# Kernel tuning notes

Measured on AMD Instinct MI355X. Metric: run time of the kernel, lower is better.

Reference implementation:

```python
import jax, jax.numpy as jnp
import numpy as np

N = 50000      # nodes
E = 250000     # edges
NG = 2500      # graphs
H = 32         # atom_dim
ND = 32        # node feature dim
ED = 16        # edge feature dim
CONV_N = 3     # message passing steps
EMB_STEPS = 3  # Set2Set processing steps


def setup_inputs() -> dict:
    key = jax.random.key(0)
    ks = jax.random.split(key, 16)
    w = lambda k, shape, s=0.05: jax.random.normal(k, shape, jnp.float32) * s
    return {
        "x": jax.random.normal(ks[0], (N, ND), jnp.float32),
        "edge_index": jax.random.randint(ks[1], (2, E), 0, N),
        "edge_attr": jax.random.normal(ks[2], (E, ED), jnp.float32),
        "batch": jnp.sort(jax.random.randint(ks[3], (N,), 0, NG)),
        "lin_w": w(ks[4], (ND, H)), "lin_b": jnp.zeros((H,), jnp.float32),
        "e_w1": w(ks[5], (ED, 2 * H)), "e_b1": jnp.zeros((2 * H,), jnp.float32),
        "e_w2": w(ks[6], (2 * H, H * H)), "e_b2": jnp.zeros((H * H,), jnp.float32),
        "gru_w_ih": w(ks[7], (3 * H, H)), "gru_w_hh": w(ks[8], (3 * H, H)),
        "gru_b_ih": jnp.zeros((3 * H,), jnp.float32), "gru_b_hh": jnp.zeros((3 * H,), jnp.float32),
        "lstm_w_ih": w(ks[9], (4 * H, 2 * H)), "lstm_w_hh": w(ks[10], (4 * H, H)),
        "lstm_b_ih": jnp.zeros((4 * H,), jnp.float32), "lstm_b_hh": jnp.zeros((4 * H,), jnp.float32),
        "pred_w": w(ks[11], (2 * H, 1)), "pred_b": jnp.zeros((1,), jnp.float32),
    }


def _mpnn_forward(x, edge_attr, lin_w, lin_b, e_w1, e_b1, e_w2, e_b2,
                  gru_w_ih, gru_w_hh, gru_b_ih, gru_b_hh,
                  lstm_w_ih, lstm_w_hh, lstm_b_ih, lstm_b_hh,
                  pred_w, pred_b, edge_index, batch):
    src, dst = edge_index[0], edge_index[1]
    # initial node embedding: relu(Linear(node_dim -> atom_dim))
    out = jax.nn.relu(x @ lin_w + lin_b)            # [N, H]
    h = out                                         # GRU hidden state [N, H]

    # edge-conditioned weights (edge MLP output is constant across conv steps)
    e_h = jax.nn.relu(edge_attr @ e_w1 + e_b1)      # [E, 2H]
    W_e = (e_h @ e_w2 + e_b2).reshape(E, H, H)      # [E, H, H]

    # mean-aggregation denominator per target node
    deg = jax.ops.segment_sum(jnp.ones((E,), out.dtype), dst, num_segments=N)
    denom = jnp.maximum(deg, 1.0)[:, None]          # [N, 1]

    for _ in range(CONV_N):
        # NNConv message: m_e = x_src @ W_e, mean-scattered to dst
        msg = jnp.einsum('eh,eho->eo', out[src], W_e)                   # [E, H]
        agg = jax.ops.segment_sum(msg, dst, num_segments=N) / denom     # [N, H]
        m = jax.nn.relu(agg)
        # single GRU cell step (seq_len=1)
        gi = m @ gru_w_ih.T + gru_b_ih              # [N, 3H]
        gh = h @ gru_w_hh.T + gru_b_hh              # [N, 3H]
        i_r, i_z, i_n = jnp.split(gi, 3, axis=-1)
        h_r, h_z, h_n = jnp.split(gh, 3, axis=-1)
        r = jax.nn.sigmoid(i_r + h_r)
        z = jax.nn.sigmoid(i_z + h_z)
        n = jnp.tanh(i_n + r * h_n)
        h = (1.0 - z) * n + z * h
        out = h

    # Set2Set pooling over graphs (only last embedding used, residual='last')
    q_star = jnp.zeros((NG, 2 * H), out.dtype)
    hl = jnp.zeros((NG, H), out.dtype)
    cl = jnp.zeros((NG, H), out.dtype)
    for _ in range(EMB_STEPS):
        g = q_star @ lstm_w_ih.T + lstm_b_ih + hl @ lstm_w_hh.T + lstm_b_hh  # [NG, 4H]
        gi_, gf_, gg_, go_ = jnp.split(g, 4, axis=-1)
        i_g = jax.nn.sigmoid(gi_)
        f_g = jax.nn.sigmoid(gf_)
        g_g = jnp.tanh(gg_)
        o_g = jax.nn.sigmoid(go_)
        cl = f_g * cl + i_g * g_g
        hl = o_g * jnp.tanh(cl)
        q = hl                                       # [NG, H]
        e = jnp.sum(out * q[batch], axis=-1)         # [N]
        e_max = jax.ops.segment_max(e, batch, num_segments=NG)
        e_exp = jnp.exp(e - e_max[batch])
        e_den = jax.ops.segment_sum(e_exp, batch, num_segments=NG)
        a = e_exp / e_den[batch]                     # softmax within each graph
        r_pool = jax.ops.segment_sum(a[:, None] * out, batch, num_segments=NG)  # [NG, H]
        q_star = jnp.concatenate([q, r_pool], axis=-1)

    pred = q_star @ pred_w + pred_b                  # [NG, 1]
    return pred.reshape(-1)


def reference(x, edge_index, edge_attr, batch, lin_w, lin_b, e_w1, e_b1, e_w2, e_b2,
              gru_w_ih, gru_w_hh, gru_b_ih, gru_b_hh,
              lstm_w_ih, lstm_w_hh, lstm_b_ih, lstm_b_hh, pred_w, pred_b):
    return _mpnn_forward(x, edge_attr, lin_w, lin_b, e_w1, e_b1, e_w2, e_b2,
                         gru_w_ih, gru_w_hh, gru_b_ih, gru_b_hh,
                         lstm_w_ih, lstm_w_hh, lstm_b_ih, lstm_b_hh,
                         pred_w, pred_b, edge_index, batch)
```

## Files before the change

### kernel.cpp

```cpp
#include <hip/hip_runtime.h>
#include <hip/hip_bf16.h>

namespace {
constexpr int kN = 50000;
constexpr int kE = 250000;
constexpr int kG = 2500;
constexpr int NB = 8;

__device__ __forceinline__ float sigmoidf_(float x) { return 1.0f / (1.0f + expf(-x)); }

__global__ void k_starts(const int* __restrict__ batch, int* __restrict__ starts) {
  int g = blockIdx.x * blockDim.x + threadIdx.x;
  if (g > kG) return;
  int lo = 0, hi = kN;
  while (lo < hi) {
    int mid = (lo + hi) >> 1;
    if (batch[mid] < g) lo = mid + 1; else hi = mid;
  }
  starts[g] = lo;
}

__global__ __launch_bounds__(256) void k_node_init(const float* __restrict__ x,
                                                   const float* __restrict__ lin_w,
                                                   const float* __restrict__ lin_b,
                                                   float* __restrict__ h) {
  __shared__ float ws[32 * 32];
  __shared__ float bs[32];
  for (int i = threadIdx.x; i < 1024; i += 256) ws[i] = lin_w[i];
  if (threadIdx.x < 32) bs[threadIdx.x] = lin_b[threadIdx.x];
  __syncthreads();
  int n = blockIdx.x * 256 + threadIdx.x;
  if (n >= kN) return;
  float xv[32];
  const float4* xp = (const float4*)(x + (size_t)n * 32);
#pragma unroll
  for (int i = 0; i < 8; ++i) {
    float4 v = xp[i];
    xv[4 * i + 0] = v.x; xv[4 * i + 1] = v.y; xv[4 * i + 2] = v.z; xv[4 * i + 3] = v.w;
  }
  float acc[32];
#pragma unroll
  for (int o = 0; o < 32; ++o) acc[o] = bs[o];
  for (int i = 0; i < 32; ++i) {
    float a = xv[i];
    const float4* wr = (const float4*)&ws[i * 32];
#pragma unroll
    for (int o4 = 0; o4 < 8; ++o4) {
      float4 w = wr[o4];
      acc[4 * o4 + 0] = fmaf(a, w.x, acc[4 * o4 + 0]);
      acc[4 * o4 + 1] = fmaf(a, w.y, acc[4 * o4 + 1]);
      acc[4 * o4 + 2] = fmaf(a, w.z, acc[4 * o4 + 2]);
      acc[4 * o4 + 3] = fmaf(a, w.w, acc[4 * o4 + 3]);
    }
  }
  float4* hp = (float4*)(h + (size_t)n * 32);
#pragma unroll
  for (int i = 0; i < 8; ++i) {
    float4 v;
    v.x = fmaxf(acc[4 * i + 0], 0.f);
    v.y = fmaxf(acc[4 * i + 1], 0.f);
    v.z = fmaxf(acc[4 * i + 2], 0.f);
    v.w = fmaxf(acc[4 * i + 3], 0.f);
    hp[i] = v;
  }
}

__global__ __launch_bounds__(256) void k_edge_h(const float* __restrict__ ea,
                                                const float* __restrict__ w1,
                                                const float* __restrict__ b1,
                                                const int* __restrict__ es_e,
                                                float* __restrict__ ehs) {
  __shared__ float ws[16 * 64];
  __shared__ float bs[64];
  for (int i = threadIdx.x; i < 1024; i += 256) ws[i] = w1[i];
  if (threadIdx.x < 64) bs[threadIdx.x] = b1[threadIdx.x];
  __syncthreads();
  int pos = blockIdx.x * 256 + threadIdx.x;
  if (pos >= kE) return;
  int e = es_e[pos];
  float av[16];
  const float4* ap = (const float4*)(ea + (size_t)e * 16);
#pragma unroll
  for (int i = 0; i < 4; ++i) {
    float4 v = ap[i];
    av[4 * i + 0] = v.x; av[4 * i + 1] = v.y; av[4 * i + 2] = v.z; av[4 * i + 3] = v.w;
  }
  float acc[64];
#pragma unroll
  for (int o = 0; o < 64; ++o) acc[o] = bs[o];
  for (int i = 0; i < 16; ++i) {
    float a = av[i];
    const float4* wr = (const float4*)&ws[i * 64];
#pragma unroll
    for (int o4 = 0; o4 < 16; ++o4) {
      float4 w = wr[o4];
      acc[4 * o4 + 0] = fmaf(a, w.x, acc[4 * o4 + 0]);
      acc[4 * o4 + 1] = fmaf(a, w.y, acc[4 * o4 + 1]);
      acc[4 * o4 + 2] = fmaf(a, w.z, acc[4 * o4 + 2]);
      acc[4 * o4 + 3] = fmaf(a, w.w, acc[4 * o4 + 3]);
    }
  }
  float4* op = (float4*)(ehs + (size_t)pos * 64);
#pragma unroll
  for (int i = 0; i < 16; ++i) {
    float4 v;
    v.x = fmaxf(acc[4 * i + 0], 0.f);
    v.y = fmaxf(acc[4 * i + 1], 0.f);
    v.z = fmaxf(acc[4 * i + 2], 0.f);
    v.w = fmaxf(acc[4 * i + 3], 0.f);
    op[i] = v;
  }
}

__global__ void k_hist2(const int* __restrict__ src, const int* __restrict__ dst,
                        int* __restrict__ cnt_s, int* __restrict__ cnt_d) {
  int e = blockIdx.x * blockDim.x + threadIdx.x;
  if (e < kE) {
    atomicAdd(&cnt_s[src[e]], 1);
    atomicAdd(&cnt_d[dst[e]], 1);
  }
}

__global__ __launch_bounds__(1024) void k_scan2(const int* __restrict__ cnt_s, int* __restrict__ offs_s,
                                                const int* __restrict__ cnt_d, int* __restrict__ offs_d) {
  const int* cnt = blockIdx.x ? cnt_d : cnt_s;
  int* offs = blockIdx.x ? offs_d : offs_s;
  __shared__ int wsum[16];
  __shared__ int wpre[16];
  __shared__ int carry_s;
  const int tid = threadIdx.x;
  const int lane = tid & 63, wv = tid >> 6;
  if (tid == 0) carry_s = 0;
  __syncthreads();
  for (int base = 0; base < kN; base += 1024) {
    int i = base + tid;
    int v = (i < kN) ? cnt[i] : 0;
    int x = v;
#pragma unroll
    for (int d = 1; d < 64; d <<= 1) {
      int t = __shfl_up(x, d, 64);
      if (lane >= d) x += t;
    }
    if (lane == 63) wsum[wv] = x;
    __syncthreads();
    if (wv == 0) {
      int y = (lane < 16) ? wsum[lane] : 0;
#pragma unroll
      for (int d = 1; d < 16; d <<= 1) {
        int t = __shfl_up(y, d, 64);
        if (lane >= d && lane < 16) y += t;
      }
      if (lane < 16) wpre[lane] = y - wsum[lane];
    }
    __syncthreads();
    int carry = carry_s;
    if (i < kN) offs[i] = carry + wpre[wv] + (x - v);
    __syncthreads();
    if (tid == 0) carry_s = carry + wpre[15] + wsum[15];
    __syncthreads();
  }
  if (tid == 0) offs[kN] = carry_s;
}

__global__ void k_scatter_s(const int* __restrict__ src, const int* __restrict__ dst,
                            const int* __restrict__ offs, int* __restrict__ cur,
                            int* __restrict__ es_e, int* __restrict__ es_dst,
                            unsigned char* __restrict__ es_nl) {
  int e = blockIdx.x * blockDim.x + threadIdx.x;
  if (e >= kE) return;
  int s = src[e];
  int pos = offs[s] + atomicAdd(&cur[s], 1);
  es_e[pos] = e;
  es_dst[pos] = dst[e];
  es_nl[pos] = (unsigned char)(s & (NB - 1));
}

__global__ void k_scatter_d(const int* __restrict__ es_dst, const int* __restrict__ offs_d,
                            int* __restrict__ cur_d, int* __restrict__ ed_pos) {
  int ei = blockIdx.x * blockDim.x + threadIdx.x;
  if (ei >= kE) return;
  int d = es_dst[ei];
  int pd = offs_d[d] + atomicAdd(&cur_d[d], 1);
  ed_pos[pd] = ei;
}

__global__ void k_w2t(const float* __restrict__ w2, float* __restrict__ w2t) {
  int i = blockIdx.x * 256 + threadIdx.x;
  if (i >= 65536) return;
  int k = i & 63, oa = i >> 6;
  int o = oa & 31, a = oa >> 5;
  w2t[i] = w2[(size_t)k * 1024 + a * 32 + o];
}

__global__ __launch_bounds__(256, 4) void k_conv5(const float* __restrict__ h,
                                                  const float* __restrict__ ehs,
                                                  const float* __restrict__ w2t,
                                                  const float* __restrict__ b2,
                                                  const unsigned char* __restrict__ es_nl,
                                                  const int* __restrict__ offs,
                                                  float* __restrict__ msgbuf) {
  __shared__ float Ts[NB][32][36];
  __shared__ float hs[NB][32];
  __shared__ float hb2[NB][32];
  const int n0 = blockIdx.x * NB;
  const int t = threadIdx.x;
  const int nloc = t >> 5, o32 = t & 31;
  hs[nloc][o32] = h[(size_t)(n0 + nloc) * 32 + o32];
  __syncthreads();
  {
    float a0 = 0.f;
#pragma unroll 8
    for (int a = 0; a < 32; ++a) a0 = fmaf(hs[nloc][a], b2[a * 32 + o32], a0);
    hb2[nloc][o32] = a0;
  }
  const int og = t >> 3;
  const int kq = t & 7;
  const int es = offs[n0], ee = offs[n0 + NB];
  const float* wp = w2t + og * 64 + kq * 4;
  const int kg = t >> 5;

  for (int kh = 0; kh < 2; ++kh) {
    float4 acc[NB];
#pragma unroll
    for (int n = 0; n < NB; ++n) acc[n] = make_float4(0.f, 0.f, 0.f, 0.f);
    const float* wph = wp + kh * 32;
#pragma unroll 2
    for (int a4 = 0; a4 < 8; ++a4) {
      const float* wa = wph + (size_t)(a4 * 4) * 2048;
      float4 w0 = *(const float4*)(wa);
      float4 w1 = *(const float4*)(wa + 2048);
      float4 w2v = *(const float4*)(wa + 4096);
      float4 w3 = *(const float4*)(wa + 6144);
#pragma unroll
      for (int n = 0; n < NB; ++n) {
        float4 hv = *(const float4*)&hs[n][a4 * 4];
        acc[n].x = fmaf(hv.x, w0.x, acc[n].x); acc[n].y = fmaf(hv.x, w0.y, acc[n].y);
        acc[n].z = fmaf(hv.x, w0.z, acc[n].z); acc[n].w = fmaf(hv.x, w0.w, acc[n].w);
        acc[n].x = fmaf(hv.y, w1.x, acc[n].x); acc[n].y = fmaf(hv.y, w1.y, acc[n].y);
        acc[n].z = fmaf(hv.y, w1.z, acc[n].z); acc[n].w = fmaf(hv.y, w1.w, acc[n].w);
        acc[n].x = fmaf(hv.z, w2v.x, acc[n].x); acc[n].y = fmaf(hv.z, w2v.y, acc[n].y);
        acc[n].z = fmaf(hv.z, w2v.z, acc[n].z); acc[n].w = fmaf(hv.z, w2v.w, acc[n].w);
        acc[n].x = fmaf(hv.w, w3.x, acc[n].x); acc[n].y = fmaf(hv.w, w3.y, acc[n].y);
        acc[n].z = fmaf(hv.w, w3.z, acc[n].z); acc[n].w = fmaf(hv.w, w3.w, acc[n].w);
      }
    }
    if (kh) __syncthreads();
#pragma unroll
    for (int n = 0; n < NB; ++n) *(float4*)&Ts[n][og][kq * 4] = acc[n];
    __syncthreads();

    for (int ei = es + kg; ei < ee; ei += 8) {
      const int nl = es_nl[ei];
      const float* ehp = ehs + (size_t)ei * 64 + kh * 32;
      float m0 = kh ? msgbuf[(size_t)ei * 32 + o32] : hb2[nl][o32];
      float m1 = 0.f, m2 = 0.f, m3 = 0.f;
      const float* tp = &Ts[nl][o32][0];
#pragma unroll
      for (int kq2 = 0; kq2 < 8; ++kq2) {
        float4 eq = *(const float4*)(ehp + kq2 * 4);
        float4 tv = *(const float4*)(tp + kq2 * 4);
        m0 = fmaf(eq.x, tv.x, m0);
        m1 = fmaf(eq.y, tv.y, m1);
        m2 = fmaf(eq.z, tv.z, m2);
        m3 = fmaf(eq.w, tv.w, m3);
      }
      msgbuf[(size_t)ei * 32 + o32] = (m0 + m1) + (m2 + m3);
    }
  }
}

__global__ __launch_bounds__(256) void k_agg(const float* __restrict__ msgbuf,
                                             const int* __restrict__ ed_pos,
                                             const int* __restrict__ offs_d,
                                             float* __restrict__ m_out) {
  int d = blockIdx.x * 8 + (threadIdx.x >> 5);
  if (d >= kN) return;
  int o = threadIdx.x & 31;
  int s = offs_d[d], e = offs_d[d + 1];
  float acc = 0.f;
  for (int base = s; base < e; base += 32) {
    int cnt = e - base; if (cnt > 32) cnt = 32;
    int p = (base + o < e) ? ed_pos[base + o] : 0;
    for (int j = 0; j < cnt; ++j) {
      int pj = __shfl(p, j, 32);
      acc += msgbuf[(size_t)pj * 32 + o];
    }
  }
  float dn = (float)(e - s);
  if (dn < 1.f) dn = 1.f;
  m_out[(size_t)d * 32 + o] = fmaxf(acc / dn, 0.f);
}

__global__ __launch_bounds__(256) void k_gru(float* __restrict__ h, const float* __restrict__ m_in,
                                             const float* __restrict__ Wih, const float* __restrict__ Whh,
                                             const float* __restrict__ bih, const float* __restrict__ bhh) {
  __shared__ float wih_s[96 * 32];
  __shared__ float whh_s[96 * 32];
  __shared__ float bih_s[96], bhh_s[96];
  for (int i = threadIdx.x; i < 96 * 32; i += 256) { wih_s[i] = Wih[i]; whh_s[i] = Whh[i]; }
  for (int i = threadIdx.x; i < 96; i += 256) { bih_s[i] = bih[i]; bhh_s[i] = bhh[i]; }
  __syncthreads();
  int n = blockIdx.x * 256 + threadIdx.x;
  if (n >= kN) return;
  float m[32], hv[32];
  const float4* ap = (const float4*)(m_in + (size_t)n * 32);
  const float4* hp = (const float4*)(h + (size_t)n * 32);
#pragma unroll
  for (int i = 0; i < 8; ++i) {
    float4 a = ap[i];
    m[4 * i + 0] = a.x; m[4 * i + 1] = a.y; m[4 * i + 2] = a.z; m[4 * i + 3] = a.w;
    float4 b = hp[i];
    hv[4 * i + 0] = b.x; hv[4 * i + 1] = b.y; hv[4 * i + 2] = b.z; hv[4 * i + 3] = b.w;
  }
  float rr[32], zz[32];
#pragma unroll 4
  for (int j = 0; j < 32; ++j) {
    float accA = bih_s[j], accB = bhh_s[j];
    const float4* wi = (const float4*)&wih_s[j * 32];
    const float4* wh = (const float4*)&whh_s[j * 32];
#pragma unroll
    for (int i = 0; i < 8; ++i) {
      float4 a = wi[i], b = wh[i];
      accA = fmaf(m[4 * i + 0], a.x, accA); accA = fmaf(m[4 * i + 1], a.y, accA);
      accA = fmaf(m[4 * i + 2], a.z, accA); accA = fmaf(m[4 * i + 3], a.w, accA);
      accB = fmaf(hv[4 * i + 0], b.x, accB); accB = fmaf(hv[4 * i + 1], b.y, accB);
      accB = fmaf(hv[4 * i + 2], b.z, accB); accB = fmaf(hv[4 * i + 3], b.w, accB);
    }
    rr[j] = sigmoidf_(accA + accB);
  }
#pragma unroll 4
  for (int j = 0; j < 32; ++j) {
    int row = 32 + j;
    float accA = bih_s[row], accB = bhh_s[row];
    const float4* wi = (const float4*)&wih_s[row * 32];
    const float4* wh = (const float4*)&whh_s[row * 32];
#pragma unroll
    for (int i = 0; i < 8; ++i) {
      float4 a = wi[i], b = wh[i];
      accA = fmaf(m[4 * i + 0], a.x, accA); accA = fmaf(m[4 * i + 1], a.y, accA);
      accA = fmaf(m[4 * i + 2], a.z, accA); accA = fmaf(m[4 * i + 3], a.w, accA);
      accB = fmaf(hv[4 * i + 0], b.x, accB); accB = fmaf(hv[4 * i + 1], b.y, accB);
      accB = fmaf(hv[4 * i + 2], b.z, accB); accB = fmaf(hv[4 * i + 3], b.w, accB);
    }
    zz[j] = sigmoidf_(accA + accB);
  }
#pragma unroll 4
  for (int j = 0; j < 32; ++j) {
    int row = 64 + j;
    float accA = bih_s[row], accB = bhh_s[row];
    const float4* wi = (const float4*)&wih_s[row * 32];
    const float4* wh = (const float4*)&whh_s[row * 32];
#pragma unroll
    for (int i = 0; i < 8; ++i) {
      float4 a = wi[i], b = wh[i];
      accA = fmaf(m[4 * i + 0], a.x, accA); accA = fmaf(m[4 * i + 1], a.y, accA);
      accA = fmaf(m[4 * i + 2], a.z, accA); accA = fmaf(m[4 * i + 3], a.w, accA);
      accB = fmaf(hv[4 * i + 0], b.x, accB); accB = fmaf(hv[4 * i + 1], b.y, accB);
      accB = fmaf(hv[4 * i + 2], b.z, accB); accB = fmaf(hv[4 * i + 3], b.w, accB);
    }
    float ng = tanhf(accA + rr[j] * accB);
    zz[j] = (1.f - zz[j]) * ng + zz[j] * hv[j];
  }
  float4* hw = (float4*)(h + (size_t)n * 32);
#pragma unroll
  for (int i = 0; i < 8; ++i)
    hw[i] = make_float4(zz[4 * i + 0], zz[4 * i + 1], zz[4 * i + 2], zz[4 * i + 3]);
}

__global__ __launch_bounds__(256) void k_s2s(const float* __restrict__ h,
                                             const int* __restrict__ starts,
                                             const float* __restrict__ lwih,
                                             const float* __restrict__ lwhh,
                                             const float* __restrict__ lbih,
                                             const float* __restrict__ lbhh,
                                             const float* __restrict__ pw,
                                             const float* __restrict__ pb,
                                             float* __restrict__ out) {
  __shared__ float wih_s[128][65];
  __shared__ float whh_s[128][33];
  __shared__ float bsum[128];
  for (int i = threadIdx.x; i < 128 * 64; i += 256) wih_s[i >> 6][i & 63] = lwih[i];
  for (int i = threadIdx.x; i < 128 * 32; i += 256) whh_s[i >> 5][i & 31] = lwhh[i];
  for (int i = threadIdx.x; i < 128; i += 256) bsum[i] = lbih[i] + lbhh[i];
  __syncthreads();
  const int g = blockIdx.x * 4 + (threadIdx.x >> 6);
  if (g >= kG) return;
  const int lane = threadIdx.x & 63;
  const int o = lane & 31;
  const int r1 = lane, r2 = lane + 64;
  const int s = starts[g], e = starts[g + 1];
  float c = 0.f, hl = 0.f, rp = 0.f;
  for (int step = 0; step < 3; ++step) {
    float v1 = bsum[r1], v2 = bsum[r2];
    for (int i = 0; i < 32; ++i) {
      float hli = __shfl(hl, i, 64);
      float rpi = __shfl(rp, i, 64);
      v1 = fmaf(wih_s[r1][i], hli, v1);
      v1 = fmaf(wih_s[r1][32 + i], rpi, v1);
      v1 = fmaf(whh_s[r1][i], hli, v1);
      v2 = fmaf(wih_s[r2][i], hli, v2);
      v2 = fmaf(wih_s[r2][32 + i], rpi, v2);
      v2 = fmaf(whh_s[r2][i], hli, v2);
    }
    float fg = sigmoidf_(__shfl(v1, 32 + o, 64));
    float og_ = sigmoidf_(__shfl(v2, 32 + o, 64));
    float ig = sigmoidf_(v1);
    float gg = tanhf(v2);
    c = fg * c + ig * gg;
    hl = og_ * tanhf(c);
    float q = __shfl(hl, o, 64);
    float mx = -3.0e38f;
    for (int nn = s; nn < e; nn += 2) {
      int n = nn + (lane >> 5);
      float val = (n < e) ? h[(size_t)n * 32 + o] * q : 0.f;
#pragma unroll
      for (int d = 16; d; d >>= 1) val += __shfl_xor(val, d, 32);
      if (n < e) mx = fmaxf(mx, val);
    }
    mx = fmaxf(mx, __shfl_xor(mx, 32, 64));
    float den = 0.f, racc = 0.f;
    for (int nn = s; nn < e; nn += 2) {
      int n = nn + (lane >> 5);
      float hvo = 0.f, val = 0.f;
      if (n < e) { hvo = h[(size_t)n * 32 + o]; val = hvo * q; }
#pragma unroll
      for (int d = 16; d; d >>= 1) val += __shfl_xor(val, d, 32);
      if (n < e) { float p = expf(val - mx); den += p; racc = fmaf(p, hvo, racc); }
    }
    den += __shfl_xor(den, 32, 64);
    racc += __shfl_xor(racc, 32, 64);
    rp = (e > s) ? racc / den : 0.f;
  }
  float acc = __shfl(hl, o, 64) * pw[o] + rp * pw[32 + o];
#pragma unroll
  for (int d = 16; d; d >>= 1) acc += __shfl_xor(acc, d, 32);
  if (lane == 0) out[g] = acc + pb[0];
}

}

extern "C" void kernel_launch(void* const* d_in, const int* in_sizes, int n_in,
                              void* d_out, int out_size, void* d_ws, size_t ws_size,
                              hipStream_t stream) {
  const float* x     = (const float*)d_in[0];
  const int*   eidx  = (const int*)d_in[1];
  const float* eattr = (const float*)d_in[2];
  const int*   batch = (const int*)d_in[3];
  const float* lin_w = (const float*)d_in[4];
  const float* lin_b = (const float*)d_in[5];
  const float* e_w1  = (const float*)d_in[6];
  const float* e_b1  = (const float*)d_in[7];
  const float* e_w2  = (const float*)d_in[8];
  const float* e_b2  = (const float*)d_in[9];
  const float* gwih  = (const float*)d_in[10];
  const float* gwhh  = (const float*)d_in[11];
  const float* gbih  = (const float*)d_in[12];
  const float* gbhh  = (const float*)d_in[13];
  const float* lwih  = (const float*)d_in[14];
  const float* lwhh  = (const float*)d_in[15];
  const float* lbih  = (const float*)d_in[16];
  const float* lbhh  = (const float*)d_in[17];
  const float* pw    = (const float*)d_in[18];
  const float* pb    = (const float*)d_in[19];
  const int* srcp = eidx;
  const int* dstp = eidx + kE;

  float* ws = (float*)d_ws;
  size_t off = 0;
  auto alloc = [&](size_t nel) {
    float* p = ws + off;
    off += (nel + 255) & ~(size_t)255;
    return p;
  };
  float* hbuf   = alloc((size_t)kN * 32);
  float* mbuf   = alloc((size_t)kN * 32);
  float* ehs    = alloc((size_t)kE * 64);
  float* msgbuf = alloc((size_t)kE * 32);
  float* w2t    = alloc(65536);
  int* starts   = (int*)alloc(kG + 1);
  int* cnt_s    = (int*)alloc(kN);
  int* cnt_d    = (int*)alloc(kN);
  int* cur_s    = (int*)alloc(kN);
  int* cur_d    = (int*)alloc(kN);
  int* offs_s   = (int*)alloc(kN + 1);
  int* offs_d   = (int*)alloc(kN + 1);
  int* es_e     = (int*)alloc(kE);
  int* es_dst   = (int*)alloc(kE);
  int* ed_pos   = (int*)alloc(kE);
  unsigned char* es_nl = (unsigned char*)alloc((kE + 3) / 4);
  if (ws_size / 4 < off) return;

  hipMemsetAsync(cnt_s, 0, (size_t)kN * 4, stream);
  hipMemsetAsync(cnt_d, 0, (size_t)kN * 4, stream);
  hipMemsetAsync(cur_s, 0, (size_t)kN * 4, stream);
  hipMemsetAsync(cur_d, 0, (size_t)kN * 4, stream);

  k_starts<<<(kG + 1 + 255) / 256, 256, 0, stream>>>(batch, starts);
  k_node_init<<<(kN + 255) / 256, 256, 0, stream>>>(x, lin_w, lin_b, hbuf);
  k_hist2<<<(kE + 255) / 256, 256, 0, stream>>>(srcp, dstp, cnt_s, cnt_d);
  k_scan2<<<2, 1024, 0, stream>>>(cnt_s, offs_s, cnt_d, offs_d);
  k_scatter_s<<<(kE + 255) / 256, 256, 0, stream>>>(srcp, dstp, offs_s, cur_s, es_e, es_dst,
                                                    es_nl);
  k_edge_h<<<(kE + 255) / 256, 256, 0, stream>>>(eattr, e_w1, e_b1, es_e, ehs);
  k_scatter_d<<<(kE + 255) / 256, 256, 0, stream>>>(es_dst, offs_d, cur_d, ed_pos);
  k_w2t<<<65536 / 256, 256, 0, stream>>>(e_w2, w2t);

  for (int step = 0; step < 3; ++step) {
    k_conv5<<<kN / NB, 256, 0, stream>>>(hbuf, ehs, w2t, e_b2, es_nl, offs_s, msgbuf);
    k_agg<<<(kN + 7) / 8, 256, 0, stream>>>(msgbuf, ed_pos, offs_d, mbuf);
    k_gru<<<(kN + 255) / 256, 256, 0, stream>>>(hbuf, mbuf, gwih, gwhh, gbih, gbhh);
  }

  k_s2s<<<(kG + 3) / 4, 256, 0, stream>>>(hbuf, starts, lwih, lwhh, lbih, lbhh, pw, pb,
                                          (float*)d_out);
}
```

Measured before the change: 979.8 us.

## Merge conv k-halves into one pass and fuse aggregation with GRU

The conv kernel now computes both 32-wide halves of the per-node transformed weights in one pass, holding twice the accumulators and a wider shared tile. Each edge message is then produced in a single 64-term dot product instead of two passes that re-read and re-write msgbuf. Separately, mean aggregation and the GRU update are fused into one kernel that stages aggregated messages in shared memory, which removes the mbuf round trip and one launch per step. The costs are higher register and shared-memory pressure (launch bound lowered to 2 waves per SIMD) and only half the threads doing GRU work in the fused kernel.

```diff
diff --git a/kernel.cpp b/kernel.cpp
--- a/kernel.cpp
+++ b/kernel.cpp
@@ -192,14 +192,14 @@
   w2t[i] = w2[(size_t)k * 1024 + a * 32 + o];
 }
 
-__global__ __launch_bounds__(256, 4) void k_conv5(const float* __restrict__ h,
+__global__ __launch_bounds__(256, 2) void k_conv6(const float* __restrict__ h,
                                                   const float* __restrict__ ehs,
                                                   const float* __restrict__ w2t,
                                                   const float* __restrict__ b2,
                                                   const unsigned char* __restrict__ es_nl,
                                                   const int* __restrict__ offs,
                                                   float* __restrict__ msgbuf) {
-  __shared__ float Ts[NB][32][36];
+  __shared__ float Ts[NB][32][68];
   __shared__ float hs[NB][32];
   __shared__ float hb2[NB][32];
   const int n0 = blockIdx.x * NB;
@@ -217,97 +217,117 @@
   const int kq = t & 7;
   const int es = offs[n0], ee = offs[n0 + NB];
   const float* wp = w2t + og * 64 + kq * 4;
+
+  float4 accA[NB], accB[NB];
+#pragma unroll
+  for (int n = 0; n < NB; ++n) {
+    accA[n] = make_float4(0.f, 0.f, 0.f, 0.f);
+    accB[n] = make_float4(0.f, 0.f, 0.f, 0.f);
+  }
+#pragma unroll 2
+  for (int a4 = 0; a4 < 8; ++a4) {
+    const float* wa = wp + (size_t)(a4 * 4) * 2048;
+    float4 wA0 = *(const float4*)(wa);
+    float4 wB0 = *(const float4*)(wa + 32);
+    float4 wA1 = *(const float4*)(wa + 2048);
+    float4 wB1 = *(const float4*)(wa + 2080);
+    float4 wA2 = *(const float4*)(wa + 4096);
+    float4 wB2 = *(const float4*)(wa + 4128);
+    float4 wA3 = *(const float4*)(wa + 6144);
+    float4 wB3 = *(const float4*)(wa + 6176);
+#pragma unroll
+    for (int n = 0; n < NB; ++n) {
+      float4 hv = *(const float4*)&hs[n][a4 * 4];
+      accA[n].x = fmaf(hv.x, wA0.x, accA[n].x); accA[n].y = fmaf(hv.x, wA0.y, accA[n].y);
+      accA[n].z = fmaf(hv.x, wA0.z, accA[n].z); accA[n].w = fmaf(hv.x, wA0.w, accA[n].w);
+      accB[n].x = fmaf(hv.x, wB0.x, accB[n].x); accB[n].y = fmaf(hv.x, wB0.y, accB[n].y);
+      accB[n].z = fmaf(hv.x, wB0.z, accB[n].z); accB[n].w = fmaf(hv.x, wB0.w, accB[n].w);
+      accA[n].x = fmaf(hv.y, wA1.x, accA[n].x); accA[n].y = fmaf(hv.y, wA1.y, accA[n].y);
+      accA[n].z = fmaf(hv.y, wA1.z, accA[n].z); accA[n].w = fmaf(hv.y, wA1.w, accA[n].w);
+      accB[n].x = fmaf(hv.y, wB1.x, accB[n].x); accB[n].y = fmaf(hv.y, wB1.y, accB[n].y);
+      accB[n].z = fmaf(hv.y, wB1.z, accB[n].z); accB[n].w = fmaf(hv.y, wB1.w, accB[n].w);
+      accA[n].x = fmaf(hv.z, wA2.x, accA[n].x); accA[n].y = fmaf(hv.z, wA2.y, accA[n].y);
+      accA[n].z = fmaf(hv.z, wA2.z, accA[n].z); accA[n].w = fmaf(hv.z, wA2.w, accA[n].w);
+      accB[n].x = fmaf(hv.z, wB2.x, accB[n].x); accB[n].y = fmaf(hv.z, wB2.y, accB[n].y);
+      accB[n].z = fmaf(hv.z, wB2.z, accB[n].z); accB[n].w = fmaf(hv.z, wB2.w, accB[n].w);
+      accA[n].x = fmaf(hv.w, wA3.x, accA[n].x); accA[n].y = fmaf(hv.w, wA3.y, accA[n].y);
+      accA[n].z = fmaf(hv.w, wA3.z, accA[n].z); accA[n].w = fmaf(hv.w, wA3.w, accA[n].w);
+      accB[n].x = fmaf(hv.w, wB3.x, accB[n].x); accB[n].y = fmaf(hv.w, wB3.y, accB[n].y);
+      accB[n].z = fmaf(hv.w, wB3.z, accB[n].z); accB[n].w = fmaf(hv.w, wB3.w, accB[n].w);
+    }
+  }
+#pragma unroll
+  for (int n = 0; n < NB; ++n) {
+    *(float4*)&Ts[n][og][kq * 4] = accA[n];
+    *(float4*)&Ts[n][og][32 + kq * 4] = accB[n];
+  }
+  __syncthreads();
+
   const int kg = t >> 5;
-
-  for (int kh = 0; kh < 2; ++kh) {
-    float4 acc[NB];
-#pragma unroll
-    for (int n = 0; n < NB; ++n) acc[n] = make_float4(0.f, 0.f, 0.f, 0.f);
-    const float* wph = wp + kh * 32;
-#pragma unroll 2
-    for (int a4 = 0; a4 < 8; ++a4) {
-      const float* wa = wph + (size_t)(a4 * 4) * 2048;
-      float4 w0 = *(const float4*)(wa);
-      float4 w1 = *(const float4*)(wa + 2048);
-      float4 w2v = *(const float4*)(wa + 4096);
-      float4 w3 = *(const float4*)(wa + 6144);
-#pragma unroll
-      for (int n = 0; n < NB; ++n) {
-        float4 hv = *(const float4*)&hs[n][a4 * 4];
-        acc[n].x = fmaf(hv.x, w0.x, acc[n].x); acc[n].y = fmaf(hv.x, w0.y, acc[n].y);
-        acc[n].z = fmaf(hv.x, w0.z, acc[n].z); acc[n].w = fmaf(hv.x, w0.w, acc[n].w);
-        acc[n].x = fmaf(hv.y, w1.x, acc[n].x); acc[n].y = fmaf(hv.y, w1.y, acc[n].y);
-        acc[n].z = fmaf(hv.y, w1.z, acc[n].z); acc[n].w = fmaf(hv.y, w1.w, acc[n].w);
-        acc[n].x = fmaf(hv.z, w2v.x, acc[n].x); acc[n].y = fmaf(hv.z, w2v.y, acc[n].y);
-        acc[n].z = fmaf(hv.z, w2v.z, acc[n].z); acc[n].w = fmaf(hv.z, w2v.w, acc[n].w);
-        acc[n].x = fmaf(hv.w, w3.x, acc[n].x); acc[n].y = fmaf(hv.w, w3.y, acc[n].y);
-        acc[n].z = fmaf(hv.w, w3.z, acc[n].z); acc[n].w = fmaf(hv.w, w3.w, acc[n].w);
-      }
-    }
-    if (kh) __syncthreads();
-#pragma unroll
-    for (int n = 0; n < NB; ++n) *(float4*)&Ts[n][og][kq * 4] = acc[n];
-    __syncthreads();
-
-    for (int ei = es + kg; ei < ee; ei += 8) {
-      const int nl = es_nl[ei];
-      const float* ehp = ehs + (size_t)ei * 64 + kh * 32;
-      float m0 = kh ? msgbuf[(size_t)ei * 32 + o32] : hb2[nl][o32];
-      float m1 = 0.f, m2 = 0.f, m3 = 0.f;
-      const float* tp = &Ts[nl][o32][0];
-#pragma unroll
-      for (int kq2 = 0; kq2 < 8; ++kq2) {
-        float4 eq = *(const float4*)(ehp + kq2 * 4);
-        float4 tv = *(const float4*)(tp + kq2 * 4);
-        m0 = fmaf(eq.x, tv.x, m0);
-        m1 = fmaf(eq.y, tv.y, m1);
-        m2 = fmaf(eq.z, tv.z, m2);
-        m3 = fmaf(eq.w, tv.w, m3);
-      }
-      msgbuf[(size_t)ei * 32 + o32] = (m0 + m1) + (m2 + m3);
-    }
-  }
-}
-
-__global__ __launch_bounds__(256) void k_agg(const float* __restrict__ msgbuf,
-                                             const int* __restrict__ ed_pos,
-                                             const int* __restrict__ offs_d,
-                                             float* __restrict__ m_out) {
-  int d = blockIdx.x * 8 + (threadIdx.x >> 5);
-  if (d >= kN) return;
-  int o = threadIdx.x & 31;
-  int s = offs_d[d], e = offs_d[d + 1];
-  float acc = 0.f;
-  for (int base = s; base < e; base += 32) {
-    int cnt = e - base; if (cnt > 32) cnt = 32;
-    int p = (base + o < e) ? ed_pos[base + o] : 0;
-    for (int j = 0; j < cnt; ++j) {
-      int pj = __shfl(p, j, 32);
-      acc += msgbuf[(size_t)pj * 32 + o];
-    }
-  }
-  float dn = (float)(e - s);
-  if (dn < 1.f) dn = 1.f;
-  m_out[(size_t)d * 32 + o] = fmaxf(acc / dn, 0.f);
-}
-
-__global__ __launch_bounds__(256) void k_gru(float* __restrict__ h, const float* __restrict__ m_in,
-                                             const float* __restrict__ Wih, const float* __restrict__ Whh,
-                                             const float* __restrict__ bih, const float* __restrict__ bhh) {
+  for (int ei = es + kg; ei < ee; ei += 8) {
+    const int nl = es_nl[ei];
+    const float* ehp = ehs + (size_t)ei * 64;
+    float m0 = hb2[nl][o32], m1 = 0.f, m2 = 0.f, m3 = 0.f;
+    const float* tp = &Ts[nl][o32][0];
+#pragma unroll
+    for (int q = 0; q < 16; ++q) {
+      float4 eq = *(const float4*)(ehp + q * 4);
+      float4 tv = *(const float4*)(tp + q * 4);
+      m0 = fmaf(eq.x, tv.x, m0);
+      m1 = fmaf(eq.y, tv.y, m1);
+      m2 = fmaf(eq.z, tv.z, m2);
+      m3 = fmaf(eq.w, tv.w, m3);
+    }
+    msgbuf[(size_t)ei * 32 + o32] = (m0 + m1) + (m2 + m3);
+  }
+}
+
+__global__ __launch_bounds__(256) void k_aggru(const float* __restrict__ msgbuf,
+                                               const int* __restrict__ ed_pos,
+                                               const int* __restrict__ offs_d,
+                                               float* __restrict__ h,
+                                               const float* __restrict__ Wih,
+                                               const float* __restrict__ Whh,
+                                               const float* __restrict__ bih,
+                                               const float* __restrict__ bhh) {
+  __shared__ float m_s[128][36];
   __shared__ float wih_s[96 * 32];
   __shared__ float whh_s[96 * 32];
   __shared__ float bih_s[96], bhh_s[96];
   for (int i = threadIdx.x; i < 96 * 32; i += 256) { wih_s[i] = Wih[i]; whh_s[i] = Whh[i]; }
   for (int i = threadIdx.x; i < 96; i += 256) { bih_s[i] = bih[i]; bhh_s[i] = bhh[i]; }
-  __syncthreads();
-  int n = blockIdx.x * 256 + threadIdx.x;
+  const int grp = threadIdx.x >> 5, o = threadIdx.x & 31;
+  const int nbase = blockIdx.x * 128;
+#pragma unroll 2
+  for (int j = 0; j < 16; ++j) {
+    int dl = grp * 16 + j;
+    int d = nbase + dl;
+    if (d < kN) {
+      int s = offs_d[d], e = offs_d[d + 1];
+      float acc = 0.f;
+      for (int base = s; base < e; base += 32) {
+        int cnt = e - base; if (cnt > 32) cnt = 32;
+        int p = (base + o < e) ? ed_pos[base + o] : 0;
+        for (int jj = 0; jj < cnt; ++jj) {
+          int pj = __shfl(p, jj, 32);
+          acc += msgbuf[(size_t)pj * 32 + o];
+        }
+      }
+      float dn = (float)(e - s);
+      if (dn < 1.f) dn = 1.f;
+      m_s[dl][o] = fmaxf(acc / dn, 0.f);
+    }
+  }
+  __syncthreads();
+  const int nl = threadIdx.x;
+  if (nl >= 128) return;
+  const int n = nbase + nl;
   if (n >= kN) return;
   float m[32], hv[32];
-  const float4* ap = (const float4*)(m_in + (size_t)n * 32);
   const float4* hp = (const float4*)(h + (size_t)n * 32);
 #pragma unroll
   for (int i = 0; i < 8; ++i) {
-    float4 a = ap[i];
+    float4 a = *(const float4*)&m_s[nl][4 * i];
     m[4 * i + 0] = a.x; m[4 * i + 1] = a.y; m[4 * i + 2] = a.z; m[4 * i + 3] = a.w;
     float4 b = hp[i];
     hv[4 * i + 0] = b.x; hv[4 * i + 1] = b.y; hv[4 * i + 2] = b.z; hv[4 * i + 3] = b.w;
@@ -473,7 +493,6 @@
     return p;
   };
   float* hbuf   = alloc((size_t)kN * 32);
-  float* mbuf   = alloc((size_t)kN * 32);
   float* ehs    = alloc((size_t)kE * 64);
   float* msgbuf = alloc((size_t)kE * 32);
   float* w2t    = alloc(65536);
@@ -506,9 +525,9 @@
   k_w2t<<<65536 / 256, 256, 0, stream>>>(e_w2, w2t);
 
   for (int step = 0; step < 3; ++step) {
-    k_conv5<<<kN / NB, 256, 0, stream>>>(hbuf, ehs, w2t, e_b2, es_nl, offs_s, msgbuf);
-    k_agg<<<(kN + 7) / 8, 256, 0, stream>>>(msgbuf, ed_pos, offs_d, mbuf);
-    k_gru<<<(kN + 255) / 256, 256, 0, stream>>>(hbuf, mbuf, gwih, gwhh, gbih, gbhh);
+    k_conv6<<<kN / NB, 256, 0, stream>>>(hbuf, ehs, w2t, e_b2, es_nl, offs_s, msgbuf);
+    k_aggru<<<(kN + 127) / 128, 256, 0, stream>>>(msgbuf, ed_pos, offs_d, hbuf,
+                                                  gwih, gwhh, gbih, gbhh);
   }
 
   k_s2s<<<(kG + 3) / 4, 256, 0, stream>>>(hbuf, starts, lwih, lwhh, lbih, lbhh, pw, pb,
```

Result: slower. 1.099 ms (+12.1%).

## Write messages in destination-sorted order and parallelize prefix scan

Applied to the files above, without the earlier changes.

Conv now writes each edge message straight to its destination-sorted slot, so the aggregation kernel reads contiguous rows instead of gathering through an index array. The two scatter kernels are merged into one that packs the destination position and local node id into a single int. The single-block serial scan becomes a three-kernel block-parallel scan, and four memsets become one. In exchange the conv stores become scattered writes, and the packing assumes fewer than 2^28 edges.

```diff
diff --git a/kernel.cpp b/kernel.cpp
--- a/kernel.cpp
+++ b/kernel.cpp
@@ -6,6 +6,7 @@
 constexpr int kE = 250000;
 constexpr int kG = 2500;
 constexpr int NB = 8;
+constexpr int NBLK = (kN + 255) / 256;
 
 __device__ __forceinline__ float sigmoidf_(float x) { return 1.0f / (1.0f + expf(-x)); }
 
@@ -121,67 +122,74 @@
   }
 }
 
-__global__ __launch_bounds__(1024) void k_scan2(const int* __restrict__ cnt_s, int* __restrict__ offs_s,
-                                                const int* __restrict__ cnt_d, int* __restrict__ offs_d) {
-  const int* cnt = blockIdx.x ? cnt_d : cnt_s;
-  int* offs = blockIdx.x ? offs_d : offs_s;
-  __shared__ int wsum[16];
-  __shared__ int wpre[16];
-  __shared__ int carry_s;
-  const int tid = threadIdx.x;
-  const int lane = tid & 63, wv = tid >> 6;
-  if (tid == 0) carry_s = 0;
-  __syncthreads();
-  for (int base = 0; base < kN; base += 1024) {
-    int i = base + tid;
-    int v = (i < kN) ? cnt[i] : 0;
-    int x = v;
-#pragma unroll
-    for (int d = 1; d < 64; d <<= 1) {
-      int t = __shfl_up(x, d, 64);
-      if (lane >= d) x += t;
-    }
-    if (lane == 63) wsum[wv] = x;
-    __syncthreads();
-    if (wv == 0) {
-      int y = (lane < 16) ? wsum[lane] : 0;
-#pragma unroll
-      for (int d = 1; d < 16; d <<= 1) {
-        int t = __shfl_up(y, d, 64);
-        if (lane >= d && lane < 16) y += t;
-      }
-      if (lane < 16) wpre[lane] = y - wsum[lane];
-    }
-    __syncthreads();
-    int carry = carry_s;
-    if (i < kN) offs[i] = carry + wpre[wv] + (x - v);
-    __syncthreads();
-    if (tid == 0) carry_s = carry + wpre[15] + wsum[15];
-    __syncthreads();
-  }
-  if (tid == 0) offs[kN] = carry_s;
-}
-
-__global__ void k_scatter_s(const int* __restrict__ src, const int* __restrict__ dst,
-                            const int* __restrict__ offs, int* __restrict__ cur,
-                            int* __restrict__ es_e, int* __restrict__ es_dst,
-                            unsigned char* __restrict__ es_nl) {
+__global__ __launch_bounds__(256) void k_scan_blk(const int* __restrict__ cnt_s, int* __restrict__ offs_s,
+                                                  const int* __restrict__ cnt_d, int* __restrict__ offs_d,
+                                                  int* __restrict__ part) {
+  const int arr = blockIdx.y;
+  const int* cnt = arr ? cnt_d : cnt_s;
+  int* offs = arr ? offs_d : offs_s;
+  __shared__ int wsum[4];
+  const int i = blockIdx.x * 256 + threadIdx.x;
+  const int lane = threadIdx.x & 63, wv = threadIdx.x >> 6;
+  int v = (i < kN) ? cnt[i] : 0;
+  int x = v;
+#pragma unroll
+  for (int d = 1; d < 64; d <<= 1) {
+    int t = __shfl_up(x, d, 64);
+    if (lane >= d) x += t;
+  }
+  if (lane == 63) wsum[wv] = x;
+  __syncthreads();
+  int pre = 0;
+#pragma unroll
+  for (int w = 0; w < 3; ++w) pre += (w < wv) ? wsum[w] : 0;
+  if (i < kN) offs[i] = pre + x - v;
+  if (threadIdx.x == 255) part[arr * 256 + blockIdx.x] = pre + x;
+}
+
+__global__ __launch_bounds__(256) void k_scan_part(int* __restrict__ part,
+                                                   int* __restrict__ offs_s,
+                                                   int* __restrict__ offs_d) {
+  const int arr = blockIdx.x;
+  int* p = part + arr * 256;
+  __shared__ int wsum[4];
+  const int i = threadIdx.x;
+  const int lane = i & 63, wv = i >> 6;
+  int v = (i < NBLK) ? p[i] : 0;
+  int x = v;
+#pragma unroll
+  for (int d = 1; d < 64; d <<= 1) {
+    int t = __shfl_up(x, d, 64);
+    if (lane >= d) x += t;
+  }
+  if (lane == 63) wsum[wv] = x;
+  __syncthreads();
+  int pre = 0;
+#pragma unroll
+  for (int w = 0; w < 3; ++w) pre += (w < wv) ? wsum[w] : 0;
+  if (i < NBLK) p[i] = pre + x - v;
+  if (i == NBLK - 1) (arr ? offs_d : offs_s)[kN] = pre + x;
+}
+
+__global__ void k_scan_add(const int* __restrict__ part, int* __restrict__ offs_s,
+                           int* __restrict__ offs_d) {
+  const int arr = blockIdx.y;
+  int* offs = arr ? offs_d : offs_s;
+  int i = blockIdx.x * 256 + threadIdx.x;
+  if (i < kN) offs[i] += part[arr * 256 + blockIdx.x];
+}
+
+__global__ void k_scatter(const int* __restrict__ src, const int* __restrict__ dst,
+                          const int* __restrict__ offs_s, const int* __restrict__ offs_d,
+                          int* __restrict__ cur_s, int* __restrict__ cur_d,
+                          int* __restrict__ es_e, int* __restrict__ es_pk) {
   int e = blockIdx.x * blockDim.x + threadIdx.x;
   if (e >= kE) return;
-  int s = src[e];
-  int pos = offs[s] + atomicAdd(&cur[s], 1);
+  int s = src[e], d = dst[e];
+  int pos = offs_s[s] + atomicAdd(&cur_s[s], 1);
+  int pd = offs_d[d] + atomicAdd(&cur_d[d], 1);
   es_e[pos] = e;
-  es_dst[pos] = dst[e];
-  es_nl[pos] = (unsigned char)(s & (NB - 1));
-}
-
-__global__ void k_scatter_d(const int* __restrict__ es_dst, const int* __restrict__ offs_d,
-                            int* __restrict__ cur_d, int* __restrict__ ed_pos) {
-  int ei = blockIdx.x * blockDim.x + threadIdx.x;
-  if (ei >= kE) return;
-  int d = es_dst[ei];
-  int pd = offs_d[d] + atomicAdd(&cur_d[d], 1);
-  ed_pos[pd] = ei;
+  es_pk[pos] = pd | ((s & (NB - 1)) << 28);
 }
 
 __global__ void k_w2t(const float* __restrict__ w2, float* __restrict__ w2t) {
@@ -196,7 +204,7 @@
                                                   const float* __restrict__ ehs,
                                                   const float* __restrict__ w2t,
                                                   const float* __restrict__ b2,
-                                                  const unsigned char* __restrict__ es_nl,
+                                                  const int* __restrict__ es_pk,
                                                   const int* __restrict__ offs,
                                                   float* __restrict__ msgbuf) {
   __shared__ float Ts[NB][32][36];
@@ -250,9 +258,11 @@
     __syncthreads();
 
     for (int ei = es + kg; ei < ee; ei += 8) {
-      const int nl = es_nl[ei];
+      const int pk = es_pk[ei];
+      const int nl = pk >> 28;
+      const int pd = pk & 0x0FFFFFFF;
       const float* ehp = ehs + (size_t)ei * 64 + kh * 32;
-      float m0 = kh ? msgbuf[(size_t)ei * 32 + o32] : hb2[nl][o32];
+      float m0 = kh ? msgbuf[(size_t)pd * 32 + o32] : hb2[nl][o32];
       float m1 = 0.f, m2 = 0.f, m3 = 0.f;
       const float* tp = &Ts[nl][o32][0];
 #pragma unroll
@@ -264,31 +274,28 @@
         m2 = fmaf(eq.z, tv.z, m2);
         m3 = fmaf(eq.w, tv.w, m3);
       }
-      msgbuf[(size_t)ei * 32 + o32] = (m0 + m1) + (m2 + m3);
+      msgbuf[(size_t)pd * 32 + o32] = (m0 + m1) + (m2 + m3);
     }
   }
 }
 
 __global__ __launch_bounds__(256) void k_agg(const float* __restrict__ msgbuf,
-                                             const int* __restrict__ ed_pos,
                                              const int* __restrict__ offs_d,
                                              float* __restrict__ m_out) {
   int d = blockIdx.x * 8 + (threadIdx.x >> 5);
   if (d >= kN) return;
   int o = threadIdx.x & 31;
   int s = offs_d[d], e = offs_d[d + 1];
-  float acc = 0.f;
-  for (int base = s; base < e; base += 32) {
-    int cnt = e - base; if (cnt > 32) cnt = 32;
-    int p = (base + o < e) ? ed_pos[base + o] : 0;
-    for (int j = 0; j < cnt; ++j) {
-      int pj = __shfl(p, j, 32);
-      acc += msgbuf[(size_t)pj * 32 + o];
-    }
-  }
+  float a0 = 0.f, a1 = 0.f;
+  int j = s;
+  for (; j + 1 < e; j += 2) {
+    a0 += msgbuf[(size_t)j * 32 + o];
+    a1 += msgbuf[(size_t)(j + 1) * 32 + o];
+  }
+  if (j < e) a0 += msgbuf[(size_t)j * 32 + o];
   float dn = (float)(e - s);
   if (dn < 1.f) dn = 1.f;
-  m_out[(size_t)d * 32 + o] = fmaxf(acc / dn, 0.f);
+  m_out[(size_t)d * 32 + o] = fmaxf((a0 + a1) / dn, 0.f);
 }
 
 __global__ __launch_bounds__(256) void k_gru(float* __restrict__ h, const float* __restrict__ m_in,
@@ -485,29 +492,29 @@
   int* offs_s   = (int*)alloc(kN + 1);
   int* offs_d   = (int*)alloc(kN + 1);
   int* es_e     = (int*)alloc(kE);
-  int* es_dst   = (int*)alloc(kE);
-  int* ed_pos   = (int*)alloc(kE);
-  unsigned char* es_nl = (unsigned char*)alloc((kE + 3) / 4);
+  int* es_pk    = (int*)alloc(kE);
+  int* part     = (int*)alloc(512);
   if (ws_size / 4 < off) return;
 
-  hipMemsetAsync(cnt_s, 0, (size_t)kN * 4, stream);
-  hipMemsetAsync(cnt_d, 0, (size_t)kN * 4, stream);
-  hipMemsetAsync(cur_s, 0, (size_t)kN * 4, stream);
-  hipMemsetAsync(cur_d, 0, (size_t)kN * 4, stream);
+  hipMemsetAsync(cnt_s, 0, (size_t)((cur_d + ((kN + 255) & ~255)) - cnt_s) * 4, stream);
 
   k_starts<<<(kG + 1 + 255) / 256, 256, 0, stream>>>(batch, starts);
   k_node_init<<<(kN + 255) / 256, 256, 0, stream>>>(x, lin_w, lin_b, hbuf);
   k_hist2<<<(kE + 255) / 256, 256, 0, stream>>>(srcp, dstp, cnt_s, cnt_d);
-  k_scan2<<<2, 1024, 0, stream>>>(cnt_s, offs_s, cnt_d, offs_d);
-  k_scatter_s<<<(kE + 255) / 256, 256, 0, stream>>>(srcp, dstp, offs_s, cur_s, es_e, es_dst,
-                                                    es_nl);
+  {
+    dim3 g(NBLK, 2);
+    k_scan_blk<<<g, 256, 0, stream>>>(cnt_s, offs_s, cnt_d, offs_d, part);
+    k_scan_part<<<2, 256, 0, stream>>>(part, offs_s, offs_d);
+    k_scan_add<<<g, 256, 0, stream>>>(part, offs_s, offs_d);
+  }
+  k_scatter<<<(kE + 255) / 256, 256, 0, stream>>>(srcp, dstp, offs_s, offs_d, cur_s, cur_d,
+                                                  es_e, es_pk);
   k_edge_h<<<(kE + 255) / 256, 256, 0, stream>>>(eattr, e_w1, e_b1, es_e, ehs);
-  k_scatter_d<<<(kE + 255) / 256, 256, 0, stream>>>(es_dst, offs_d, cur_d, ed_pos);
   k_w2t<<<65536 / 256, 256, 0, stream>>>(e_w2, w2t);
 
   for (int step = 0; step < 3; ++step) {
-    k_conv5<<<kN / NB, 256, 0, stream>>>(hbuf, ehs, w2t, e_b2, es_nl, offs_s, msgbuf);
-    k_agg<<<(kN + 7) / 8, 256, 0, stream>>>(msgbuf, ed_pos, offs_d, mbuf);
+    k_conv5<<<kN / NB, 256, 0, stream>>>(hbuf, ehs, w2t, e_b2, es_pk, offs_s, msgbuf);
+    k_agg<<<(kN + 7) / 8, 256, 0, stream>>>(msgbuf, offs_d, mbuf);
     k_gru<<<(kN + 255) / 256, 256, 0, stream>>>(hbuf, mbuf, gwih, gwhh, gbih, gbhh);
   }
 
```

New measurement: 915.8 us. 1.07x faster.
